# Performance work log

Hardware: AMD Instinct MI355X
Metric: run time of the kernel (lower is better)

## Reference

```python
import jax, jax.numpy as jnp
import numpy as np

D_MODEL, D_STATE, D_CONV, EXPAND = 1024, 16, 4, 2
D_INNER = EXPAND * D_MODEL           # 2048
DT_RANK = D_MODEL // 16              # 64
BATCH, SEQLEN = 2, 2048


def setup_inputs() -> dict:
    key = jax.random.key(0)
    ks = jax.random.split(key, 10)
    s = 0.02
    hidden_states = jax.random.normal(ks[0], (BATCH, SEQLEN, D_MODEL), jnp.float32)
    in_proj_w = jax.random.normal(ks[1], (2 * D_INNER, D_MODEL), jnp.float32) * s
    conv_w = jax.random.normal(ks[2], (D_INNER, 1, D_CONV), jnp.float32) * 0.3
    conv_b = jax.random.normal(ks[3], (D_INNER,), jnp.float32) * 0.1
    x_proj_w = jax.random.normal(ks[4], (DT_RANK + 2 * D_STATE, D_INNER), jnp.float32) * s
    dt_init_std = DT_RANK ** -0.5
    dt_proj_w = jax.random.uniform(ks[5], (D_INNER, DT_RANK), jnp.float32,
                                   minval=-dt_init_std, maxval=dt_init_std)
    # bias = inverse-softplus of dt sampled log-uniform in [1e-3, 1e-1]
    dt = jnp.exp(jax.random.uniform(ks[6], (D_INNER,), jnp.float32)
                 * (np.log(0.1) - np.log(0.001)) + np.log(0.001))
    dt = jnp.clip(dt, 1e-4, None)
    dt_proj_b = dt + jnp.log(-jnp.expm1(-dt))
    # A = repeat(arange(1, d_state+1), 'n -> d n')
    A_log = jnp.log(jnp.tile(jnp.arange(1, D_STATE + 1, dtype=jnp.float32), (D_INNER, 1)))
    Dp = jnp.ones((D_INNER,), jnp.float32)
    out_proj_w = jax.random.normal(ks[7], (D_MODEL, D_INNER), jnp.float32) * s
    return {
        'hidden_states': hidden_states, 'in_proj_w': in_proj_w,
        'conv_w': conv_w, 'conv_b': conv_b, 'x_proj_w': x_proj_w,
        'dt_proj_w': dt_proj_w, 'dt_proj_b': dt_proj_b,
        'A_log': A_log, 'D': Dp, 'out_proj_w': out_proj_w,
    }


def _mamba_fwd(hidden_states, in_proj_w, conv_w, conv_b, x_proj_w,
               dt_proj_w, dt_proj_b, A_log, D, out_proj_w):
    d_inner = in_proj_w.shape[0] // 2
    d_conv = conv_w.shape[-1]
    dt_rank = dt_proj_w.shape[1]
    d_state = A_log.shape[1]
    b = hidden_states.shape[0]

    # in_proj then split into x / z gate branches  -> [B, L, d_inner] each
    xz = hidden_states @ in_proj_w.T
    x, z = jnp.split(xz, 2, axis=-1)

    # depthwise causal conv1d + SiLU (pad left d_conv-1 == padding=d_conv-1 then trim)
    xc = x.transpose(0, 2, 1)                       # [B, d_inner, L]
    xc = jax.lax.conv_general_dilated(
        xc, conv_w, window_strides=(1,), padding=[(d_conv - 1, 0)],
        dimension_numbers=('NCH', 'OIH', 'NCH'), feature_group_count=d_inner)
    xl = jax.nn.silu(xc + conv_b[None, :, None]).transpose(0, 2, 1)  # [B, L, d_inner]

    # x_proj -> dt, B, C
    x_dbl = xl @ x_proj_w.T                         # [B, L, dt_rank + 2*d_state]
    dt, Bm, Cm = jnp.split(x_dbl, [dt_rank, dt_rank + d_state], axis=-1)
    delta = jax.nn.softplus(dt @ dt_proj_w.T + dt_proj_b)  # [B, L, d_inner]

    A = -jnp.exp(A_log)                             # [d_inner, d_state]

    def step(h, inputs):
        u_t, d_t, b_t, c_t = inputs  # [B,d_inner], [B,d_inner], [B,d_state], [B,d_state]
        dA = jnp.exp(d_t[..., None] * A)                      # [B, d_inner, d_state]
        h = dA * h + (d_t * u_t)[..., None] * b_t[:, None, :]
        y_t = jnp.einsum('bdn,bn->bd', h, c_t)
        return h, y_t

    h0 = jnp.zeros((b, d_inner, d_state), hidden_states.dtype)
    xs = (xl.transpose(1, 0, 2), delta.transpose(1, 0, 2),
          Bm.transpose(1, 0, 2), Cm.transpose(1, 0, 2))
    _, ys = jax.lax.scan(step, h0, xs)              # ys: [L, B, d_inner]
    y = ys.transpose(1, 0, 2)

    y = y + xl * D                                  # skip (D) term
    y = y * jax.nn.silu(z)                          # gate
    return y @ out_proj_w.T                         # [B, L, d_model]


def reference(hidden_states, in_proj_w, conv_w, conv_b, x_proj_w,
              dt_proj_w, dt_proj_b, A_log, D, out_proj_w):
    return _mamba_fwd(hidden_states, in_proj_w, conv_w, conv_b, x_proj_w,
                      dt_proj_w, dt_proj_b, A_log, D, out_proj_w)
```

## Files before the change

### kernel.cpp

```cpp
#include <hip/hip_runtime.h>

#define D_MODEL 1024
#define D_STATE 16
#define D_CONV  4
#define D_INNER 2048
#define DT_RANK 64
#define BATCH   2
#define SEQLEN  2048
#define NTOK    (BATCH * SEQLEN)
#define NCH     64
#define LC      (SEQLEN / NCH)
#define XKS     8
#define XNC     96


__device__ __forceinline__ float bf2f(unsigned short v) {
    union { unsigned int u; float f; } c; c.u = ((unsigned int)v) << 16; return c.f;
}
__device__ __forceinline__ unsigned short f2bf(float f) {
    union { unsigned int u; float f; } c; c.f = f;
    unsigned int r = c.u + 0x7FFF + ((c.u >> 16) & 1);
    return (unsigned short)(r >> 16);
}

__device__ __forceinline__ int sniff_bf(const void* Dp) {
    return (((const unsigned int*)Dp)[0] == 0x3F803F80u) ? 1 : 0;
}

__device__ __forceinline__ float ldF(const void* p, size_t idx, int isbf) {
    return isbf ? bf2f(((const unsigned short*)p)[idx]) : ((const float*)p)[idx];
}
__device__ __forceinline__ void ld16f(const float* p, float* o) {
#pragma unroll
    for (int q = 0; q < 4; q++) {
        float4 v = *(const float4*)(p + 4 * q);
        o[4 * q + 0] = v.x; o[4 * q + 1] = v.y; o[4 * q + 2] = v.z; o[4 * q + 3] = v.w;
    }
}

typedef __attribute__((ext_vector_type(8))) __bf16 bf16x8;
typedef __attribute__((ext_vector_type(4))) float  f32x4;

__device__ void probe_dmap_block(int t, int* __restrict__ dmap)
{
    __shared__ alignas(16) unsigned short PAs[16 * 32];
    __shared__ alignas(16) unsigned short PBs[16 * 32];
    const int q = (t & 63) >> 4, l15 = t & 15;

    if (t < 64)
        for (int idx = t; idx < 512; idx += 64) {
            PAs[idx] = f2bf((float)(idx >> 5));
            PBs[idx] = f2bf(0.03125f);
        }
    __syncthreads();
    f32x4 acc1 = {0.f, 0.f, 0.f, 0.f};
    if (t < 64) {
        bf16x8 a1 = *(const bf16x8*)&PAs[l15 * 32 + q * 8];
        bf16x8 b1 = *(const bf16x8*)&PBs[l15 * 32 + q * 8];
        acc1 = __builtin_amdgcn_mfma_f32_16x16x32_bf16(a1, b1, acc1, 0, 0, 0);
    }
    __syncthreads();
    if (t < 64)
        for (int idx = t; idx < 512; idx += 64) {
            PAs[idx] = f2bf(0.03125f);
            PBs[idx] = f2bf((float)(idx >> 5));
        }
    __syncthreads();
    if (t < 64) {
        bf16x8 a2 = *(const bf16x8*)&PAs[l15 * 32 + q * 8];
        bf16x8 b2 = *(const bf16x8*)&PBs[l15 * 32 + q * 8];
        f32x4 acc2 = {0.f, 0.f, 0.f, 0.f};
        acc2 = __builtin_amdgcn_mfma_f32_16x16x32_bf16(a2, b2, acc2, 0, 0, 0);
#pragma unroll
        for (int r = 0; r < 4; r++) {
            int ma = (int)(acc1[r] + 0.5f);
            int nb = (int)(acc2[r] + 0.5f);
            if (ma < 0 || ma > 15 || nb < 0 || nb > 15) { ma = q * 4 + r; nb = l15; }
            dmap[t * 4 + r] = ma | (nb << 4);
        }
    }
}

#define CVT_N0 (NTOK * D_MODEL)
#define CVT_N1 (2 * D_INNER * D_MODEL)
#define CVT_N2 (D_MODEL * D_INNER)
#define CVT_N3 (D_INNER * DT_RANK)
#define CVT_TOT (CVT_N0 + CVT_N1 + CVT_N2 + CVT_N3)

__device__ __forceinline__ void cvt8(const void* in, unsigned short* out,
                                     size_t e0, int isbf)
{
    if (isbf) {
        *(uint4*)(out + e0) = *(const uint4*)((const unsigned short*)in + e0);
    } else {
        const float* f = (const float*)in + e0;
        float4 a = *(const float4*)f;
        float4 b = *(const float4*)(f + 4);
        ushort4 o0 = { f2bf(a.x), f2bf(a.y), f2bf(a.z), f2bf(a.w) };
        ushort4 o1 = { f2bf(b.x), f2bf(b.y), f2bf(b.z), f2bf(b.w) };
        *(ushort4*)(out + e0)     = o0;
        *(ushort4*)(out + e0 + 4) = o1;
    }
}

__launch_bounds__(256)
__global__ void cvt_all(const void* __restrict__ hid, const void* __restrict__ ipw,
                        const void* __restrict__ opw, const void* __restrict__ dtw,
                        unsigned short* __restrict__ hidB, unsigned short* __restrict__ ipwB,
                        unsigned short* __restrict__ opwB, unsigned short* __restrict__ dtwB,
                        const void* __restrict__ Dp, int* __restrict__ dmap)
{
    if (blockIdx.x == 0) probe_dmap_block(threadIdx.x, dmap);

    const int isbf = sniff_bf(Dp);
    size_t e = ((size_t)blockIdx.x * 256 + threadIdx.x) * 8;
    if (e < CVT_N0) { cvt8(hid, hidB, e, isbf); return; }
    e -= CVT_N0;
    if (e < CVT_N1) { cvt8(ipw, ipwB, e, isbf); return; }
    e -= CVT_N1;
    if (e < CVT_N2) { cvt8(opw, opwB, e, isbf); return; }
    e -= CVT_N2;
    if (e < CVT_N3) { cvt8(dtw, dtwB, e, isbf); }
}

__device__ __forceinline__ void gl2lds16(const void* g, void* l) {
    __builtin_amdgcn_global_load_lds(
        (const __attribute__((address_space(1))) unsigned int*)g,
        (__attribute__((address_space(3))) unsigned int*)l,
        16, 0, 0);
}

__device__ __forceinline__ void stage_half(const unsigned short* __restrict__ G,
                                           int grow0, int K, int k0,
                                           unsigned short* ldsAB, int half, int t)
{
    const int r8  = t >> 3;
    const int c8  = t & 7;
    const int swz = (c8 ^ (r8 & 7)) << 3;
#pragma unroll
    for (int j = 0; j < 2; j++) {
        const int row = half * 128 + j * 64 + r8;
        gl2lds16(&G[(size_t)(grow0 + row) * K + k0 + swz],
                 &ldsAB[row * 64 + c8 * 8]);
    }
}

__device__ __forceinline__ bf16x8 ldsfrag(const unsigned short* p, int row, int slot) {
    return *(const bf16x8*)&p[row * 64 + ((slot ^ (row & 7)) << 3)];
}

__launch_bounds__(512)
__global__ void gemm1_8ph(const unsigned short* __restrict__ A,
                          const unsigned short* __restrict__ B,
                          float* __restrict__ C,
                          int M, int N, int K,
                          const int* __restrict__ dmap)
{
    extern __shared__ __align__(16) unsigned short lds[];
    unsigned short* A0l = lds;
    unsigned short* B0l = lds + 16384;
    unsigned short* A1l = lds + 32768;
    unsigned short* B1l = lds + 49152;

    const int t    = threadIdx.x;
    const int lane = t & 63;
    const int w    = t >> 6;
    const int wm   = (w >> 2) * 128, wn = (w & 3) * 64;
    const int q    = lane >> 4, l15 = lane & 15;

    const int nbn  = N >> 8;
    const int nwg  = (M >> 8) * nbn;
    const int orig = blockIdx.x;
    const int wg   = (orig & 7) * (nwg >> 3) + (orig >> 3);
    const int bm   = wg / nbn, bn = wg % nbn;
    const int m0   = bm << 8, n0 = bn << 8;
    const int NT   = K >> 6;

    int mp[4];
#pragma unroll
    for (int r = 0; r < 4; r++) mp[r] = dmap[lane * 4 + r];

    f32x4 acc[8][4];
#pragma unroll
    for (int i = 0; i < 8; i++)
#pragma unroll
        for (int j = 0; j < 4; j++) acc[i][j] = (f32x4){0.f, 0.f, 0.f, 0.f};

    stage_half(B, n0, K, 0, B0l, 0, t);
    stage_half(B, n0, K, 0, B0l, 1, t);
    stage_half(A, m0, K, 0, A0l, 0, t);
    stage_half(A, m0, K, 0, A0l, 1, t);
    {
        const int k1 = (NT > 1 ? 64 : 0);
        stage_half(B, n0, K, k1, B1l, 0, t);
        stage_half(B, n0, K, k1, B1l, 1, t);
    }
    asm volatile("s_waitcnt vmcnt(4)" ::: "memory");
    __builtin_amdgcn_s_barrier();

#pragma unroll 2
    for (int tt = 0; tt < NT; ++tt) {
        const int p = tt & 1;
        const unsigned short* Ac = p ? A1l : A0l;
        const unsigned short* Bc = p ? B1l : B0l;
        unsigned short* Anx = p ? A0l : A1l;
        unsigned short* Bnx = p ? B1l : B0l;
        const int kA = (tt + 1 < NT ? tt + 1 : 0) << 6;
        const int kB = (tt + 2 < NT ? tt + 2 : 0) << 6;

        bf16x8 af[4][2], b0r[2][2], b1r[2][2];

#pragma unroll
        for (int i = 0; i < 4; i++)
#pragma unroll
            for (int ks = 0; ks < 2; ks++)
                af[i][ks] = ldsfrag(Ac, wm + i * 16 + l15, ks * 4 + q);
#pragma unroll
        for (int j = 0; j < 2; j++)
#pragma unroll
            for (int ks = 0; ks < 2; ks++)
                b0r[j][ks] = ldsfrag(Bc, wn + j * 16 + l15, ks * 4 + q);
        stage_half(A, m0, K, kA, Anx, 0, t);
        asm volatile("" ::: "memory");
        __builtin_amdgcn_s_barrier();
        __builtin_amdgcn_s_setprio(1);
#pragma unroll
        for (int i = 0; i < 4; i++)
#pragma unroll
            for (int j = 0; j < 2; j++)
#pragma unroll
                for (int ks = 0; ks < 2; ks++)
                    acc[i][j] = __builtin_amdgcn_mfma_f32_16x16x32_bf16(
                        af[i][ks], b0r[j][ks], acc[i][j], 0, 0, 0);
        __builtin_amdgcn_s_setprio(0);
        asm volatile("" ::: "memory");
        __builtin_amdgcn_s_barrier();

#pragma unroll
        for (int j = 0; j < 2; j++)
#pragma unroll
            for (int ks = 0; ks < 2; ks++)
                b1r[j][ks] = ldsfrag(Bc, wn + 32 + j * 16 + l15, ks * 4 + q);
        stage_half(A, m0, K, kA, Anx, 1, t);
        asm volatile("" ::: "memory");
        __builtin_amdgcn_s_barrier();
        __builtin_amdgcn_s_setprio(1);
#pragma unroll
        for (int i = 0; i < 4; i++)
#pragma unroll
            for (int j = 0; j < 2; j++)
#pragma unroll
                for (int ks = 0; ks < 2; ks++)
                    acc[i][2 + j] = __builtin_amdgcn_mfma_f32_16x16x32_bf16(
                        af[i][ks], b1r[j][ks], acc[i][2 + j], 0, 0, 0);
        __builtin_amdgcn_s_setprio(0);
        asm volatile("" ::: "memory");
        __builtin_amdgcn_s_barrier();

#pragma unroll
        for (int i = 0; i < 4; i++)
#pragma unroll
            for (int ks = 0; ks < 2; ks++)
                af[i][ks] = ldsfrag(Ac, wm + 64 + i * 16 + l15, ks * 4 + q);
        stage_half(B, n0, K, kB, Bnx, 0, t);
        asm volatile("" ::: "memory");
        __builtin_amdgcn_s_barrier();
        __builtin_amdgcn_s_setprio(1);
#pragma unroll
        for (int i = 0; i < 4; i++)
#pragma unroll
            for (int j = 0; j < 2; j++)
#pragma unroll
                for (int ks = 0; ks < 2; ks++)
                    acc[4 + i][2 + j] = __builtin_amdgcn_mfma_f32_16x16x32_bf16(
                        af[i][ks], b1r[j][ks], acc[4 + i][2 + j], 0, 0, 0);
        __builtin_amdgcn_s_setprio(0);
        asm volatile("" ::: "memory");
        __builtin_amdgcn_s_barrier();

        stage_half(B, n0, K, kB, Bnx, 1, t);
        asm volatile("" ::: "memory");
        __builtin_amdgcn_s_barrier();
        __builtin_amdgcn_s_setprio(1);
#pragma unroll
        for (int i = 0; i < 4; i++)
#pragma unroll
            for (int j = 0; j < 2; j++)
#pragma unroll
                for (int ks = 0; ks < 2; ks++)
                    acc[4 + i][j] = __builtin_amdgcn_mfma_f32_16x16x32_bf16(
                        af[i][ks], b0r[j][ks], acc[4 + i][j], 0, 0, 0);
        __builtin_amdgcn_s_setprio(0);
        asm volatile("s_waitcnt vmcnt(4)" ::: "memory");
        __builtin_amdgcn_s_barrier();
    }

#pragma unroll
    for (int i = 0; i < 8; i++) {
#pragma unroll
        for (int r = 0; r < 4; r++) {
            const int mo = mp[r] & 15, no = mp[r] >> 4;
            const int m = m0 + wm + i * 16 + mo;
#pragma unroll
            for (int j = 0; j < 4; j++) {
                const int n = n0 + wn + j * 16 + no;
                C[(size_t)m * N + n] = acc[i][j][r];
            }
        }
    }
}

__device__ __forceinline__ void stage_op(const unsigned short* __restrict__ A,
                                         const unsigned short* __restrict__ B,
                                         int m0, int n0, int K, int k0,
                                         unsigned short* Al, unsigned short* Bl, int t)
{
    const int r   = t >> 3;
    const int c8  = t & 7;
    const int swz = (c8 ^ (r & 7)) << 3;
#pragma unroll
    for (int j = 0; j < 4; j++) {
        const int row = j * 32 + r;
        gl2lds16(&A[(size_t)(m0 + row) * K + k0 + swz], &Al[row * 64 + c8 * 8]);
    }
#pragma unroll
    for (int j = 0; j < 2; j++) {
        const int row = j * 32 + r;
        gl2lds16(&B[(size_t)(n0 + row) * K + k0 + swz], &Bl[row * 64 + c8 * 8]);
    }
}

__launch_bounds__(256)
__global__ void gemm_op_2ph(const unsigned short* __restrict__ A,
                            const unsigned short* __restrict__ B,
                            float* __restrict__ C,
                            const int* __restrict__ dmap)
{
    constexpr int M = NTOK, N = D_MODEL, K = D_INNER;
    constexpr int NT = K / 64;
    __shared__ alignas(16) unsigned short Al[2][128 * 64];
    __shared__ alignas(16) unsigned short Bl[2][64 * 64];

    const int t    = threadIdx.x;
    const int lane = t & 63;
    const int w    = t >> 6;
    const int wm   = (w >> 1) * 64, wn = (w & 1) * 32;
    const int q    = lane >> 4, l15 = lane & 15;

    const int nbn  = N / 64;
    const int nwg  = (M / 128) * nbn;
    const int orig = blockIdx.x;
    const int wg   = (orig & 7) * (nwg >> 3) + (orig >> 3);
    const int bm   = wg / nbn, bn = wg % nbn;
    const int m0   = bm * 128, n0 = bn * 64;

    int mp[4];
#pragma unroll
    for (int r = 0; r < 4; r++) mp[r] = dmap[lane * 4 + r];

    f32x4 acc[4][2];
#pragma unroll
    for (int i = 0; i < 4; i++)
#pragma unroll
        for (int j = 0; j < 2; j++) acc[i][j] = (f32x4){0.f, 0.f, 0.f, 0.f};

    stage_op(A, B, m0, n0, K, 0, Al[0], Bl[0], t);
    asm volatile("s_waitcnt vmcnt(0)" ::: "memory");
    __builtin_amdgcn_s_barrier();

#pragma unroll 2
    for (int tt = 0; tt < NT - 1; ++tt) {
        const int cur = tt & 1;
        stage_op(A, B, m0, n0, K, (tt + 1) * 64, Al[cur ^ 1], Bl[cur ^ 1], t);

        bf16x8 af[4][2], bfr[2][2];
#pragma unroll
        for (int i = 0; i < 4; i++)
#pragma unroll
            for (int ks = 0; ks < 2; ks++)
                af[i][ks] = ldsfrag(Al[cur], wm + i * 16 + l15, ks * 4 + q);
#pragma unroll
        for (int j = 0; j < 2; j++)
#pragma unroll
            for (int ks = 0; ks < 2; ks++)
                bfr[j][ks] = ldsfrag(Bl[cur], wn + j * 16 + l15, ks * 4 + q);
        __builtin_amdgcn_s_setprio(1);
#pragma unroll
        for (int i = 0; i < 4; i++)
#pragma unroll
            for (int j = 0; j < 2; j++)
#pragma unroll
                for (int ks = 0; ks < 2; ks++)
                    acc[i][j] = __builtin_amdgcn_mfma_f32_16x16x32_bf16(
                        af[i][ks], bfr[j][ks], acc[i][j], 0, 0, 0);
        __builtin_amdgcn_s_setprio(0);
        asm volatile("s_waitcnt vmcnt(0)" ::: "memory");
        __builtin_amdgcn_s_barrier();
    }

    {
        const int cur = (NT - 1) & 1;
        bf16x8 af[4][2], bfr[2][2];
#pragma unroll
        for (int i = 0; i < 4; i++)
#pragma unroll
            for (int ks = 0; ks < 2; ks++)
                af[i][ks] = ldsfrag(Al[cur], wm + i * 16 + l15, ks * 4 + q);
#pragma unroll
        for (int j = 0; j < 2; j++)
#pragma unroll
            for (int ks = 0; ks < 2; ks++)
                bfr[j][ks] = ldsfrag(Bl[cur], wn + j * 16 + l15, ks * 4 + q);
#pragma unroll
        for (int i = 0; i < 4; i++)
#pragma unroll
            for (int j = 0; j < 2; j++)
#pragma unroll
                for (int ks = 0; ks < 2; ks++)
                    acc[i][j] = __builtin_amdgcn_mfma_f32_16x16x32_bf16(
                        af[i][ks], bfr[j][ks], acc[i][j], 0, 0, 0);
    }

#pragma unroll
    for (int i = 0; i < 4; i++) {
#pragma unroll
        for (int r = 0; r < 4; r++) {
            const int mo = mp[r] & 15, no = mp[r] >> 4;
            const int m = m0 + wm + i * 16 + mo;
#pragma unroll
            for (int j = 0; j < 2; j++) {
                const int n = n0 + wn + j * 16 + no;
                C[(size_t)m * N + n] = acc[i][j][r];
            }
        }
    }
}

__launch_bounds__(256)
__global__ void gemm_dt(const unsigned short* __restrict__ A,
                        const unsigned short* __restrict__ B,
                        float* __restrict__ C,
                        const int* __restrict__ dmap,
                        const void* __restrict__ bias,
                        const void* __restrict__ Dp)
{
    constexpr int M = NTOK, N = D_INNER, K = DT_RANK;
    __shared__ alignas(16) unsigned short Al[128 * 64];
    __shared__ alignas(16) unsigned short Bl[128 * 64];

    const int t    = threadIdx.x;
    const int lane = t & 63;
    const int w    = t >> 6;
    const int wm   = (w >> 1) * 64, wn = (w & 1) * 64;
    const int q    = lane >> 4, l15 = lane & 15;

    const int nbn  = N / 128;
    const int nwg  = (M / 128) * nbn;
    const int orig = blockIdx.x;
    const int wg   = (orig & 7) * (nwg >> 3) + (orig >> 3);
    const int bm   = wg / nbn, bn = wg % nbn;
    const int m0   = bm * 128, n0 = bn * 128;

    int mp[4];
#pragma unroll
    for (int r = 0; r < 4; r++) mp[r] = dmap[lane * 4 + r];

    {
        const int r   = t >> 3;
        const int c8  = t & 7;
        const int swz = (c8 ^ (r & 7)) << 3;
#pragma unroll
        for (int j = 0; j < 4; j++) {
            const int row = j * 32 + r;
            gl2lds16(&A[(size_t)(m0 + row) * K + swz], &Al[row * 64 + c8 * 8]);
            gl2lds16(&B[(size_t)(n0 + row) * K + swz], &Bl[row * 64 + c8 * 8]);
        }
    }
    asm volatile("s_waitcnt vmcnt(0)" ::: "memory");
    __builtin_amdgcn_s_barrier();

    f32x4 acc[4][4];
#pragma unroll
    for (int i = 0; i < 4; i++)
#pragma unroll
        for (int j = 0; j < 4; j++) acc[i][j] = (f32x4){0.f, 0.f, 0.f, 0.f};

    bf16x8 af[4][2], bfr[4][2];
#pragma unroll
    for (int i = 0; i < 4; i++)
#pragma unroll
        for (int ks = 0; ks < 2; ks++)
            af[i][ks] = ldsfrag(Al, wm + i * 16 + l15, ks * 4 + q);
#pragma unroll
    for (int j = 0; j < 4; j++)
#pragma unroll
        for (int ks = 0; ks < 2; ks++)
            bfr[j][ks] = ldsfrag(Bl, wn + j * 16 + l15, ks * 4 + q);
#pragma unroll
    for (int i = 0; i < 4; i++)
#pragma unroll
        for (int j = 0; j < 4; j++)
#pragma unroll
            for (int ks = 0; ks < 2; ks++)
                acc[i][j] = __builtin_amdgcn_mfma_f32_16x16x32_bf16(
                    af[i][ks], bfr[j][ks], acc[i][j], 0, 0, 0);

    const int isbf = sniff_bf(Dp);
#pragma unroll
    for (int i = 0; i < 4; i++) {
#pragma unroll
        for (int r = 0; r < 4; r++) {
            const int mo = mp[r] & 15, no = mp[r] >> 4;
            const int m = m0 + wm + i * 16 + mo;
#pragma unroll
            for (int j = 0; j < 4; j++) {
                const int n = n0 + wn + j * 16 + no;
                float v = acc[i][j][r] + ldF(bias, n, isbf);
                v = fmaxf(v, 0.f) + __logf(1.f + __expf(-fabsf(v)));
                C[(size_t)m * N + n] = v;
            }
        }
    }
}

__launch_bounds__(256)
__global__ void xproj_splitk(const float* __restrict__ A,
                             const float* __restrict__ B,
                             float* __restrict__ part)
{
    __shared__ alignas(16) float As[16][68];
    __shared__ alignas(16) float Bs[16][68];
    const int t  = threadIdx.x;
    const int m0 = blockIdx.y * 64, n0 = blockIdx.x * 64;
    const int koff = blockIdx.z * (D_INNER / XKS);
    const int lr = t >> 2;
    const int lk = (t & 3) * 4;
    const int tm = t >> 4, tn = t & 15;

    float acc[4][4];
#pragma unroll
    for (int i = 0; i < 4; i++)
#pragma unroll
        for (int j = 0; j < 4; j++) acc[i][j] = 0.f;

    for (int k0 = koff; k0 < koff + D_INNER / XKS; k0 += 16) {
        float av[4], bv[4];
        {
            const int m = m0 + lr;
            float4 p = *(const float4*)&A[(size_t)m * D_INNER + k0 + lk];
            av[0] = p.x; av[1] = p.y; av[2] = p.z; av[3] = p.w;
        }
        {
            const int n = n0 + lr;
            if (n < XNC) {
                float4 p = *(const float4*)&B[(size_t)n * D_INNER + k0 + lk];
                bv[0] = p.x; bv[1] = p.y; bv[2] = p.z; bv[3] = p.w;
            } else { bv[0] = bv[1] = bv[2] = bv[3] = 0.f; }
        }
        __syncthreads();
#pragma unroll
        for (int i = 0; i < 4; i++) { As[lk + i][lr] = av[i]; Bs[lk + i][lr] = bv[i]; }
        __syncthreads();

#pragma unroll
        for (int kk = 0; kk < 16; kk++) {
            float4 a = *(const float4*)&As[kk][tm * 4];
            float4 b = *(const float4*)&Bs[kk][tn * 4];
            float aa[4] = { a.x, a.y, a.z, a.w };
            float bb[4] = { b.x, b.y, b.z, b.w };
#pragma unroll
            for (int i = 0; i < 4; i++)
#pragma unroll
                for (int j = 0; j < 4; j++) acc[i][j] = fmaf(aa[i], bb[j], acc[i][j]);
        }
    }

    float* out = part + (size_t)blockIdx.z * NTOK * XNC;
#pragma unroll
    for (int i = 0; i < 4; i++) {
        const int m = m0 + tm * 4 + i;
#pragma unroll
        for (int j = 0; j < 4; j++) {
            const int n = n0 + tn * 4 + j;
            if (n < XNC) out[(size_t)m * XNC + n] = acc[i][j];
        }
    }
}

__launch_bounds__(256)
__global__ void xproj_reduce(const float* __restrict__ part, float* __restrict__ xdbl,
                             unsigned short* __restrict__ xdt)
{
    const int idx = blockIdx.x * 256 + threadIdx.x;
    float s = 0.f;
#pragma unroll
    for (int z = 0; z < XKS; z++) s += part[(size_t)z * NTOK * XNC + idx];
    xdbl[idx] = s;
    const int m = idx / XNC;
    const int col = idx - m * XNC;
    if (col < 64) xdt[m * 64 + col] = f2bf(s);
}

__launch_bounds__(256)
__global__ void conv_silu(const float* __restrict__ xz,
                          const void* __restrict__ conv_w,
                          const void* __restrict__ conv_b,
                          float* __restrict__ xl,
                          const void* __restrict__ Dp)
{
    const int isbf = sniff_bf(Dp);
    const int gid = blockIdx.x * 256 + threadIdx.x;
    const int dq  = gid & (D_INNER / 4 - 1);
    const int tg  = gid >> 9;
    const int d0  = dq * 4;
    const int tok0 = tg * 4;
    const int l0  = tok0 & (SEQLEN - 1);

    float w[4][4], bias[4];
#pragma unroll
    for (int dd = 0; dd < 4; dd++) {
        bias[dd] = ldF(conv_b, d0 + dd, isbf);
#pragma unroll
        for (int j = 0; j < 4; j++) w[dd][j] = ldF(conv_w, (d0 + dd) * 4 + j, isbf);
    }

    float4 x[7];
    const float* rowp = xz + (size_t)tok0 * (2 * D_INNER) + d0;
#pragma unroll
    for (int k = 0; k < 7; k++) {
        const int off = k - 3;
        if (l0 + off >= 0)
            x[k] = *(const float4*)(rowp + (ptrdiff_t)off * (2 * D_INNER));
        else
            x[k] = (float4){0.f, 0.f, 0.f, 0.f};
    }

#pragma unroll
    for (int tn = 0; tn < 4; tn++) {
        float a0 = bias[0], a1 = bias[1], a2 = bias[2], a3 = bias[3];
#pragma unroll
        for (int j = 0; j < 4; j++) {
            const float4 v = x[tn + j];
            a0 = fmaf(v.x, w[0][j], a0);
            a1 = fmaf(v.y, w[1][j], a1);
            a2 = fmaf(v.z, w[2][j], a2);
            a3 = fmaf(v.w, w[3][j], a3);
        }
        float4 o;
        o.x = a0 / (1.f + __expf(-a0));
        o.y = a1 / (1.f + __expf(-a1));
        o.z = a2 / (1.f + __expf(-a2));
        o.w = a3 / (1.f + __expf(-a3));
        *(float4*)&xl[(size_t)(tok0 + tn) * D_INNER + d0] = o;
    }
}

__device__ __forceinline__ void mk_dA(float dv, const float An[16], int pw, float* dA)
{
    if (pw) {
        const float E = __expf(dv * An[0]);
        dA[0] = E;
        const float E2 = E * E;          dA[1] = E2;
        const float E4 = E2 * E2;        dA[3] = E4;
        const float E8 = E4 * E4;        dA[7] = E8;
        dA[2]  = E2 * E;
        dA[4]  = E4 * E;   dA[5]  = E4 * E2;  dA[6]  = dA[5] * E;
        dA[8]  = E8 * E;   dA[9]  = E8 * E2;  dA[10] = dA[9] * E;
        dA[11] = E8 * E4;  dA[12] = dA[11] * E;
        dA[13] = dA[11] * E2; dA[14] = dA[13] * E; dA[15] = E8 * E8;
    } else {
#pragma unroll
        for (int n = 0; n < 16; n++) dA[n] = __expf(dv * An[n]);
    }
}

__device__ __forceinline__ int chk_pw(const float An[16])
{
    int pw = 1;
#pragma unroll
    for (int n = 1; n < 16; n++)
        pw = pw && (fabsf(An[n] - (float)(n + 1) * An[0]) <= 3e-4f * (float)(n + 1));
    return pw;
}

__device__ __forceinline__ void scan_step(float h[16], float dv, float uv,
                                          const float Bv[16], const float An[16], int pw)
{
    float dA[16]; mk_dA(dv, An, pw, dA);
    const float du = dv * uv;
#pragma unroll
    for (int n = 0; n < 16; n++) h[n] = fmaf(dA[n], h[n], du * Bv[n]);
}

__device__ __forceinline__ float scan_step_y(float h[16], float dv, float uv,
                                             const float Bv[16], const float Cv[16],
                                             const float An[16], int pw, float Dd)
{
    float dA[16]; mk_dA(dv, An, pw, dA);
    const float du = dv * uv;
    float s[16];
#pragma unroll
    for (int n = 0; n < 16; n++) {
        h[n] = fmaf(dA[n], h[n], du * Bv[n]);
        s[n] = h[n] * Cv[n];
    }
#pragma unroll
    for (int n = 0; n < 8; n++) s[n] += s[n + 8];
#pragma unroll
    for (int n = 0; n < 4; n++) s[n] += s[n + 4];
    s[0] += s[2]; s[1] += s[3];
    return s[0] + s[1] + uv * Dd;
}

__launch_bounds__(256)
__global__ void scan_chunk(const float* __restrict__ dlt,
                           const float* __restrict__ xl,
                           const float* __restrict__ xdbl,
                           const void* __restrict__ A_log,
                           float* __restrict__ S,
                           float* __restrict__ sumD,
                           const void* __restrict__ Dp)
{
    const int isbf = sniff_bf(Dp);
    const int t  = threadIdx.x;
    const int dg = blockIdx.x & 7;
    const int c  = (blockIdx.x >> 3) & (NCH - 1);
    const int b  = blockIdx.x >> 9;
    const int d  = dg * 256 + t;

    float An[16], h[16];
#pragma unroll
    for (int n = 0; n < 16; n++) {
        An[n] = -expf(ldF(A_log, d * 16 + n, isbf));
        h[n] = 0.f;
    }
    const int pw = chk_pw(An);
    float sd = 0.f;
    const size_t r0 = (size_t)b * SEQLEN + c * LC;

    float dv0 = dlt[r0 * D_INNER + d];
    float uv0 = xl [r0 * D_INNER + d];
    float Bv0[16]; ld16f(&xdbl[r0 * 96 + 64], Bv0);

    for (int i = 0; i < LC; i += 2) {
        const size_t r1 = r0 + i + 1;
        float dv1 = dlt[r1 * D_INNER + d];
        float uv1 = xl [r1 * D_INNER + d];
        float Bv1[16]; ld16f(&xdbl[r1 * 96 + 64], Bv1);

        scan_step(h, dv0, uv0, Bv0, An, pw);
        sd += dv0;

        const size_t r2 = r0 + ((i + 2 < LC) ? (i + 2) : (i + 1));
        dv0 = dlt[r2 * D_INNER + d];
        uv0 = xl [r2 * D_INNER + d];
        ld16f(&xdbl[r2 * 96 + 64], Bv0);

        scan_step(h, dv1, uv1, Bv1, An, pw);
        sd += dv1;
    }

    const size_t base = (((size_t)b * NCH + c) * 16) * D_INNER + d;
#pragma unroll
    for (int n = 0; n < 16; n++) S[base + (size_t)n * D_INNER] = h[n];
    sumD[((size_t)b * NCH + c) * D_INNER + d] = sd;
}

__launch_bounds__(256)
__global__ void scan_combine(float* __restrict__ S,
                             const float* __restrict__ sumD,
                             const void* __restrict__ A_log,
                             const void* __restrict__ Dp)
{
    const int isbf = sniff_bf(Dp);
    const int g = blockIdx.x * 256 + threadIdx.x;
    const int d = g & (D_INNER - 1);
    const int n = (g >> 11) & 15;
    const int b = g >> 15;
    const float An = -expf(ldF(A_log, d * 16 + n, isbf));

    float hs = 0.f;
    float Sc = S[(((size_t)b * NCH + 0) * 16 + n) * D_INNER + d];
    float sd = sumD[((size_t)b * NCH + 0) * D_INNER + d];
    for (int c = 0; c < NCH; c++) {
        const int cn = (c + 1 < NCH) ? c + 1 : c;
        const float Scn = S[(((size_t)b * NCH + cn) * 16 + n) * D_INNER + d];
        const float sdn = sumD[((size_t)b * NCH + cn) * D_INNER + d];
        S[(((size_t)b * NCH + c) * 16 + n) * D_INNER + d] = hs;
        hs = fmaf(__expf(An * sd), hs, Sc);
        Sc = Scn; sd = sdn;
    }
}

__launch_bounds__(256)
__global__ void scan_apply(const float* __restrict__ dlt,
                           const float* __restrict__ xl,
                           const float* __restrict__ xdbl,
                           const float* __restrict__ xz,
                           const void* __restrict__ A_log,
                           const void* __restrict__ Dp,
                           const float* __restrict__ S,
                           unsigned short* __restrict__ yg)
{
    const int isbf = sniff_bf(Dp);
    const int t  = threadIdx.x;
    const int dg = blockIdx.x & 7;
    const int c  = (blockIdx.x >> 3) & (NCH - 1);
    const int b  = blockIdx.x >> 9;
    const int d  = dg * 256 + t;

    float An[16], h[16];
    const size_t base = (((size_t)b * NCH + c) * 16) * D_INNER + d;
#pragma unroll
    for (int n = 0; n < 16; n++) {
        An[n] = -expf(ldF(A_log, d * 16 + n, isbf));
        h[n] = S[base + (size_t)n * D_INNER];
    }
    const int pw = chk_pw(An);
    const float Dd = ldF(Dp, d, isbf);
    const size_t r0 = (size_t)b * SEQLEN + c * LC;

    float dv0 = dlt[r0 * D_INNER + d];
    float uv0 = xl [r0 * D_INNER + d];
    float zv0 = xz [r0 * (2 * D_INNER) + D_INNER + d];
    float Bv0[16], Cv0[16];
    ld16f(&xdbl[r0 * 96 + 64], Bv0);
    ld16f(&xdbl[r0 * 96 + 80], Cv0);

    for (int i = 0; i < LC; i += 2) {
        const size_t ra = r0 + i + 1;
        float dv1 = dlt[ra * D_INNER + d];
        float uv1 = xl [ra * D_INNER + d];
        float zv1 = xz [ra * (2 * D_INNER) + D_INNER + d];
        float Bv1[16], Cv1[16];
        ld16f(&xdbl[ra * 96 + 64], Bv1);
        ld16f(&xdbl[ra * 96 + 80], Cv1);

        {
            const float yv = scan_step_y(h, dv0, uv0, Bv0, Cv0, An, pw, Dd);
            yg[(r0 + i) * D_INNER + d] = f2bf(yv * (zv0 / (1.f + __expf(-zv0))));
        }

        const size_t rb = r0 + ((i + 2 < LC) ? (i + 2) : (i + 1));
        dv0 = dlt[rb * D_INNER + d];
        uv0 = xl [rb * D_INNER + d];
        zv0 = xz [rb * (2 * D_INNER) + D_INNER + d];
        ld16f(&xdbl[rb * 96 + 64], Bv0);
        ld16f(&xdbl[rb * 96 + 80], Cv0);

        {
            const float yv = scan_step_y(h, dv1, uv1, Bv1, Cv1, An, pw, Dd);
            yg[ra * D_INNER + d] = f2bf(yv * (zv1 / (1.f + __expf(-zv1))));
        }
    }
}

extern "C" void kernel_launch(void* const* d_in, const int* in_sizes, int n_in,
                              void* d_out, int out_size, void* d_ws, size_t ws_size,
                              hipStream_t stream)
{
    const void* hidden     = d_in[0];
    const void* in_proj_w  = d_in[1];
    const void* conv_w     = d_in[2];
    const void* conv_b     = d_in[3];
    const void* x_proj_w   = d_in[4];
    const void* dt_proj_w  = d_in[5];
    const void* dt_proj_b  = d_in[6];
    const void* A_log      = d_in[7];
    const void* Dp         = d_in[8];
    const void* out_proj_w = d_in[9];

    char* ws = (char*)d_ws;
    float*          xz   = (float*)(ws);
    float*          xl   = (float*)(ws + 67108864ull);
    float*          xdbl = (float*)(ws + 100663296ull);
    float*          dlt  = (float*)(ws + 102236160ull);
    unsigned short* yg   = (unsigned short*)(ws + 135790592ull);
    unsigned short* opwB = (unsigned short*)(ws + 152567808ull);
    unsigned short* xdt  = (unsigned short*)(ws + 156762112ull);
    unsigned short* dtwB = (unsigned short*)(ws + 157286400ull);
    float*          S    = (float*)(ws + 169345280ull);
    float*          sumD = (float*)(ws + 186122496ull);
    int*            dmap = (int*)  (ws + 187171072ull);
    unsigned short* hidB  = (unsigned short*)(ws + 102236160ull);
    unsigned short* ipwB  = (unsigned short*)(ws + 102236160ull + 8388608ull);
    float*          xpart = (float*)(ws + 102236160ull);

    dim3 blk(256);

    cvt_all<<<dim3(CVT_TOT / (256 * 8)), blk, 0, stream>>>(
        hidden, in_proj_w, out_proj_w, dt_proj_w, hidB, ipwB, opwB, dtwB, Dp, dmap);

    hipFuncSetAttribute((const void*)gemm1_8ph,
                        hipFuncAttributeMaxDynamicSharedMemorySize, 131072);
    gemm1_8ph<<<dim3((NTOK / 256) * (2 * D_INNER / 256)), dim3(512), 131072, stream>>>(
        hidB, ipwB, xz, NTOK, 2 * D_INNER, D_MODEL, dmap);

    conv_silu<<<dim3((NTOK / 4) * (D_INNER / 4) / 256), blk, 0, stream>>>(
        xz, conv_w, conv_b, xl, Dp);

    xproj_splitk<<<dim3(2, 64, XKS), blk, 0, stream>>>(
        xl, (const float*)x_proj_w, xpart);
    xproj_reduce<<<dim3(NTOK * XNC / 256), blk, 0, stream>>>(xpart, xdbl, xdt);

    gemm_dt<<<dim3((NTOK / 128) * (D_INNER / 128)), blk, 0, stream>>>(
        xdt, dtwB, dlt, dmap, dt_proj_b, Dp);

    scan_chunk<<<dim3(BATCH * NCH * (D_INNER / 256)), blk, 0, stream>>>(
        dlt, xl, xdbl, A_log, S, sumD, Dp);
    scan_combine<<<dim3(BATCH * 16 * D_INNER / 256), blk, 0, stream>>>(
        S, sumD, A_log, Dp);
    scan_apply<<<dim3(BATCH * NCH * (D_INNER / 256)), blk, 0, stream>>>(
        dlt, xl, xdbl, xz, A_log, Dp, S, yg);

    gemm_op_2ph<<<dim3((NTOK / 128) * (D_MODEL / 64)), blk, 0, stream>>>(
        yg, opwB, (float*)d_out, dmap);
}
```

Baseline: 312.0 us.

## Run x_proj GEMM on bf16 MFMA instead of fp32 FMA split-K

```diff
diff --git a/kernel.cpp b/kernel.cpp
--- a/kernel.cpp
+++ b/kernel.cpp
@@ -85,7 +85,8 @@
 #define CVT_N1 (2 * D_INNER * D_MODEL)
 #define CVT_N2 (D_MODEL * D_INNER)
 #define CVT_N3 (D_INNER * DT_RANK)
-#define CVT_TOT (CVT_N0 + CVT_N1 + CVT_N2 + CVT_N3)
+#define CVT_N4 (XNC * D_INNER)
+#define CVT_TOT (CVT_N0 + CVT_N1 + CVT_N2 + CVT_N3 + CVT_N4)
 
 __device__ __forceinline__ void cvt8(const void* in, unsigned short* out,
                                      size_t e0, int isbf)
@@ -106,8 +107,10 @@
 __launch_bounds__(256)
 __global__ void cvt_all(const void* __restrict__ hid, const void* __restrict__ ipw,
                         const void* __restrict__ opw, const void* __restrict__ dtw,
+                        const void* __restrict__ xpw,
                         unsigned short* __restrict__ hidB, unsigned short* __restrict__ ipwB,
                         unsigned short* __restrict__ opwB, unsigned short* __restrict__ dtwB,
+                        unsigned short* __restrict__ xpwB,
                         const void* __restrict__ Dp, int* __restrict__ dmap)
 {
     if (blockIdx.x == 0) probe_dmap_block(threadIdx.x, dmap);
@@ -120,7 +123,9 @@
     e -= CVT_N1;
     if (e < CVT_N2) { cvt8(opw, opwB, e, isbf); return; }
     e -= CVT_N2;
-    if (e < CVT_N3) { cvt8(dtw, dtwB, e, isbf); }
+    if (e < CVT_N3) { cvt8(dtw, dtwB, e, isbf); return; }
+    e -= CVT_N3;
+    if (e < CVT_N4) { cvt8(xpw, xpwB, e, isbf); }
 }
 
 __device__ __forceinline__ void gl2lds16(const void* g, void* l) {
@@ -437,6 +442,129 @@
 }
 
 __launch_bounds__(256)
+__global__ void gemm_xp(const unsigned short* __restrict__ A,
+                        const unsigned short* __restrict__ B,
+                        float* __restrict__ part,
+                        const int* __restrict__ dmap)
+{
+    constexpr int K  = D_INNER;
+    constexpr int KC = K / XKS;
+    constexpr int NT = KC / 64;
+    __shared__ alignas(16) unsigned short Al[2][128 * 64];
+    __shared__ alignas(16) unsigned short Bl[2][96 * 64];
+
+    const int t    = threadIdx.x;
+    const int lane = t & 63;
+    const int w    = t >> 6;
+    const int wm   = (w >> 1) * 64, wn = (w & 1) * 48;
+    const int q    = lane >> 4, l15 = lane & 15;
+
+    const int m0   = blockIdx.x * 128;
+    const int z    = blockIdx.y;
+    const int koff = z * KC;
+
+    int mp[4];
+#pragma unroll
+    for (int r = 0; r < 4; r++) mp[r] = dmap[lane * 4 + r];
+
+    f32x4 acc[4][3];
+#pragma unroll
+    for (int i = 0; i < 4; i++)
+#pragma unroll
+        for (int j = 0; j < 3; j++) acc[i][j] = (f32x4){0.f, 0.f, 0.f, 0.f};
+
+    auto stage_xp = [&](int k0, unsigned short* Ald, unsigned short* Bld) {
+        const int r   = t >> 3;
+        const int c8  = t & 7;
+        const int swz = (c8 ^ (r & 7)) << 3;
+#pragma unroll
+        for (int j = 0; j < 4; j++) {
+            const int row = j * 32 + r;
+            gl2lds16(&A[(size_t)(m0 + row) * K + koff + k0 + swz],
+                     &Ald[row * 64 + c8 * 8]);
+        }
+#pragma unroll
+        for (int j = 0; j < 3; j++) {
+            const int row = j * 32 + r;
+            gl2lds16(&B[(size_t)row * K + koff + k0 + swz],
+                     &Bld[row * 64 + c8 * 8]);
+        }
+    };
+
+    stage_xp(0, Al[0], Bl[0]);
+    asm volatile("s_waitcnt vmcnt(0)" ::: "memory");
+    __builtin_amdgcn_s_barrier();
+
+#pragma unroll
+    for (int tt = 0; tt < NT - 1; ++tt) {
+        const int cur = tt & 1;
+        stage_xp((tt + 1) * 64, Al[cur ^ 1], Bl[cur ^ 1]);
+
+        bf16x8 af[4][2], bfr[3][2];
+#pragma unroll
+        for (int i = 0; i < 4; i++)
+#pragma unroll
+            for (int ks = 0; ks < 2; ks++)
+                af[i][ks] = ldsfrag(Al[cur], wm + i * 16 + l15, ks * 4 + q);
+#pragma unroll
+        for (int j = 0; j < 3; j++)
+#pragma unroll
+            for (int ks = 0; ks < 2; ks++)
+                bfr[j][ks] = ldsfrag(Bl[cur], wn + j * 16 + l15, ks * 4 + q);
+        __builtin_amdgcn_s_setprio(1);
+#pragma unroll
+        for (int i = 0; i < 4; i++)
+#pragma unroll
+            for (int j = 0; j < 3; j++)
+#pragma unroll
+                for (int ks = 0; ks < 2; ks++)
+                    acc[i][j] = __builtin_amdgcn_mfma_f32_16x16x32_bf16(
+                        af[i][ks], bfr[j][ks], acc[i][j], 0, 0, 0);
+        __builtin_amdgcn_s_setprio(0);
+        asm volatile("s_waitcnt vmcnt(0)" ::: "memory");
+        __builtin_amdgcn_s_barrier();
+    }
+
+    {
+        const int cur = (NT - 1) & 1;
+        bf16x8 af[4][2], bfr[3][2];
+#pragma unroll
+        for (int i = 0; i < 4; i++)
+#pragma unroll
+            for (int ks = 0; ks < 2; ks++)
+                af[i][ks] = ldsfrag(Al[cur], wm + i * 16 + l15, ks * 4 + q);
+#pragma unroll
+        for (int j = 0; j < 3; j++)
+#pragma unroll
+            for (int ks = 0; ks < 2; ks++)
+                bfr[j][ks] = ldsfrag(Bl[cur], wn + j * 16 + l15, ks * 4 + q);
+#pragma unroll
+        for (int i = 0; i < 4; i++)
+#pragma unroll
+            for (int j = 0; j < 3; j++)
+#pragma unroll
+                for (int ks = 0; ks < 2; ks++)
+                    acc[i][j] = __builtin_amdgcn_mfma_f32_16x16x32_bf16(
+                        af[i][ks], bfr[j][ks], acc[i][j], 0, 0, 0);
+    }
+
+    float* out = part + (size_t)z * NTOK * XNC;
+#pragma unroll
+    for (int i = 0; i < 4; i++) {
+#pragma unroll
+        for (int r = 0; r < 4; r++) {
+            const int mo = mp[r] & 15, no = mp[r] >> 4;
+            const int m = m0 + wm + i * 16 + mo;
+#pragma unroll
+            for (int j = 0; j < 3; j++) {
+                const int n = wn + j * 16 + no;
+                out[(size_t)m * XNC + n] = acc[i][j][r];
+            }
+        }
+    }
+}
+
+__launch_bounds__(256)
 __global__ void gemm_dt(const unsigned short* __restrict__ A,
                         const unsigned short* __restrict__ B,
                         float* __restrict__ C,
@@ -524,70 +652,6 @@
 }
 
 __launch_bounds__(256)
-__global__ void xproj_splitk(const float* __restrict__ A,
-                             const float* __restrict__ B,
-                             float* __restrict__ part)
-{
-    __shared__ alignas(16) float As[16][68];
-    __shared__ alignas(16) float Bs[16][68];
-    const int t  = threadIdx.x;
-    const int m0 = blockIdx.y * 64, n0 = blockIdx.x * 64;
-    const int koff = blockIdx.z * (D_INNER / XKS);
-    const int lr = t >> 2;
-    const int lk = (t & 3) * 4;
-    const int tm = t >> 4, tn = t & 15;
-
-    float acc[4][4];
-#pragma unroll
-    for (int i = 0; i < 4; i++)
-#pragma unroll
-        for (int j = 0; j < 4; j++) acc[i][j] = 0.f;
-
-    for (int k0 = koff; k0 < koff + D_INNER / XKS; k0 += 16) {
-        float av[4], bv[4];
-        {
-            const int m = m0 + lr;
-            float4 p = *(const float4*)&A[(size_t)m * D_INNER + k0 + lk];
-            av[0] = p.x; av[1] = p.y; av[2] = p.z; av[3] = p.w;
-        }
-        {
-            const int n = n0 + lr;
-            if (n < XNC) {
-                float4 p = *(const float4*)&B[(size_t)n * D_INNER + k0 + lk];
-                bv[0] = p.x; bv[1] = p.y; bv[2] = p.z; bv[3] = p.w;
-            } else { bv[0] = bv[1] = bv[2] = bv[3] = 0.f; }
-        }
-        __syncthreads();
-#pragma unroll
-        for (int i = 0; i < 4; i++) { As[lk + i][lr] = av[i]; Bs[lk + i][lr] = bv[i]; }
-        __syncthreads();
-
-#pragma unroll
-        for (int kk = 0; kk < 16; kk++) {
-            float4 a = *(const float4*)&As[kk][tm * 4];
-            float4 b = *(const float4*)&Bs[kk][tn * 4];
-            float aa[4] = { a.x, a.y, a.z, a.w };
-            float bb[4] = { b.x, b.y, b.z, b.w };
-#pragma unroll
-            for (int i = 0; i < 4; i++)
-#pragma unroll
-                for (int j = 0; j < 4; j++) acc[i][j] = fmaf(aa[i], bb[j], acc[i][j]);
-        }
-    }
-
-    float* out = part + (size_t)blockIdx.z * NTOK * XNC;
-#pragma unroll
-    for (int i = 0; i < 4; i++) {
-        const int m = m0 + tm * 4 + i;
-#pragma unroll
-        for (int j = 0; j < 4; j++) {
-            const int n = n0 + tn * 4 + j;
-            if (n < XNC) out[(size_t)m * XNC + n] = acc[i][j];
-        }
-    }
-}
-
-__launch_bounds__(256)
 __global__ void xproj_reduce(const float* __restrict__ part, float* __restrict__ xdbl,
                              unsigned short* __restrict__ xdt)
 {
@@ -606,6 +670,7 @@
                           const void* __restrict__ conv_w,
                           const void* __restrict__ conv_b,
                           float* __restrict__ xl,
+                          unsigned short* __restrict__ xlB,
                           const void* __restrict__ Dp)
 {
     const int isbf = sniff_bf(Dp);
@@ -652,6 +717,8 @@
         o.z = a2 / (1.f + __expf(-a2));
         o.w = a3 / (1.f + __expf(-a3));
         *(float4*)&xl[(size_t)(tok0 + tn) * D_INNER + d0] = o;
+        ushort4 ob = { f2bf(o.x), f2bf(o.y), f2bf(o.z), f2bf(o.w) };
+        *(ushort4*)&xlB[(size_t)(tok0 + tn) * D_INNER + d0] = ob;
     }
 }
 
@@ -879,17 +946,20 @@
     unsigned short* opwB = (unsigned short*)(ws + 152567808ull);
     unsigned short* xdt  = (unsigned short*)(ws + 156762112ull);
     unsigned short* dtwB = (unsigned short*)(ws + 157286400ull);
+    unsigned short* xpwB = (unsigned short*)(ws + 157548544ull);
     float*          S    = (float*)(ws + 169345280ull);
     float*          sumD = (float*)(ws + 186122496ull);
     int*            dmap = (int*)  (ws + 187171072ull);
     unsigned short* hidB  = (unsigned short*)(ws + 102236160ull);
     unsigned short* ipwB  = (unsigned short*)(ws + 102236160ull + 8388608ull);
-    float*          xpart = (float*)(ws + 102236160ull);
+    unsigned short* xlB   = (unsigned short*)(ws + 102236160ull);
+    float*          xpart = (float*)(ws + 102236160ull + 16777216ull);
 
     dim3 blk(256);
 
     cvt_all<<<dim3(CVT_TOT / (256 * 8)), blk, 0, stream>>>(
-        hidden, in_proj_w, out_proj_w, dt_proj_w, hidB, ipwB, opwB, dtwB, Dp, dmap);
+        hidden, in_proj_w, out_proj_w, dt_proj_w, x_proj_w,
+        hidB, ipwB, opwB, dtwB, xpwB, Dp, dmap);
 
     hipFuncSetAttribute((const void*)gemm1_8ph,
                         hipFuncAttributeMaxDynamicSharedMemorySize, 131072);
@@ -897,10 +967,9 @@
         hidB, ipwB, xz, NTOK, 2 * D_INNER, D_MODEL, dmap);
 
     conv_silu<<<dim3((NTOK / 4) * (D_INNER / 4) / 256), blk, 0, stream>>>(
-        xz, conv_w, conv_b, xl, Dp);
-
-    xproj_splitk<<<dim3(2, 64, XKS), blk, 0, stream>>>(
-        xl, (const float*)x_proj_w, xpart);
+        xz, conv_w, conv_b, xl, xlB, Dp);
+
+    gemm_xp<<<dim3(NTOK / 128, XKS), blk, 0, stream>>>(xlB, xpwB, xpart, dmap);
     xproj_reduce<<<dim3(NTOK * XNC / 256), blk, 0, stream>>>(xpart, xdbl, xdt);
 
     gemm_dt<<<dim3((NTOK / 128) * (D_INNER / 128)), blk, 0, stream>>>(
```

After: 291.5 us. -6.6%, faster.
